# Optimization experiments

Measured on AMD Instinct MI355X. Metric: run time of the kernel, lower is better.

## Reference

```python
import jax, jax.numpy as jnp
import numpy as np

BIG_NUMBER = 1e7   # repo constant used to mask padded adjacency slots
MAX_ITERS = 32     # params['flow_iters']


def _build_graph(B, N, D, valid_deg, seed=0):
    """Random d-regular-ish graph: each valid slot d holds a permutation of nodes,
    so every node has exactly `valid_deg` in-edges. in_indices[b,v,d] = (b,u,s)
    such that adj[b,u,s] == v. Padded slots (d >= valid_deg) hold the sentinel N
    and their in_indices point to a padded (near-zero-weight) flow entry."""
    rng = np.random.default_rng(seed)
    adj = np.full((B, N, D), N, dtype=np.int32)
    in_idx = np.zeros((B, N, D, 3), dtype=np.int32)
    in_idx[..., 0] = np.arange(B, dtype=np.int32)[:, None, None]
    in_idx[..., 2] = valid_deg  # padded slots -> flow[b, 0, valid_deg] (weight ~ 0)
    for b in range(B):
        for d in range(valid_deg):
            perm = rng.permutation(N).astype(np.int32)
            adj[b, :, d] = perm                      # edge u -> perm[u] via slot d
            inv = np.argsort(perm).astype(np.int32)  # inv[v] = u with perm[u] == v
            in_idx[b, :, d, 1] = inv
            in_idx[b, :, d, 2] = d
    return jnp.asarray(adj), jnp.asarray(in_idx)


def setup_inputs():
    B, N, D, VALID = 4, 100000, 16, 12
    key = jax.random.key(0)
    k1, k2 = jax.random.split(key)
    adj_lst, in_indices = _build_graph(B, N, D, VALID)
    return {
        "flow_proportions": jax.random.normal(k1, (B, N, D), dtype=jnp.float32),
        "demands": jax.random.normal(k2, (B, N, 1), dtype=jnp.float32),
        "adj_lst": adj_lst,
        "in_indices": in_indices,
        "num_nodes": N,
    }


def reference(flow_proportions, demands, adj_lst, in_indices, num_nodes):
    # --- masked softmax over neighbor slots (padded slots get -BIG_NUMBER) ---
    mask = (adj_lst == num_nodes).astype(flow_proportions.dtype)   # [B,N,D]
    masked = flow_proportions - BIG_NUMBER * mask
    weights = jax.nn.softmax(masked, axis=-1)                      # normalized_weights

    # --- mcf_solver: iterate flow <- weights * relu(inflow - demand) ---
    bidx = in_indices[..., 0]   # [B,N,D] batch index
    src = in_indices[..., 1]    # [B,N,D] source node of d-th in-edge
    slot = in_indices[..., 2]   # [B,N,D] slot of this node in source's adj list

    def step(flow, _):
        # gather incoming edge flows, sum -> inflow per node [B,N,1]
        inflow = flow[bidx, src, slot].sum(axis=-1, keepdims=True)
        new_flow = weights * jax.nn.relu(inflow - demands)
        return new_flow, None

    flow, _ = jax.lax.scan(step, jnp.zeros_like(weights), None, length=MAX_ITERS)
    # flow_cost (loss) = sum over nodes/slots of cost_fn(flow) = flow**2 here:
    # flow_cost = jnp.sum(flow * flow, axis=(1, 2))
    return flow
```

## Files before the change

kernel.cpp:

```cpp
#include <hip/hip_runtime.h>

#define DEG 16
#define E12 12
#define MAX_ITERS 32
#define BLK 1024
#define LDSF 25600
#define JMAX 96

typedef float f32x4 __attribute__((ext_vector_type(4)));

__device__ __forceinline__ float ld_sc0(const float* p) {
    return __hip_atomic_load((float*)p, __ATOMIC_RELAXED, __HIP_MEMORY_SCOPE_AGENT);
}
__device__ __forceinline__ void st_sc0(float* p, float v) {
    __hip_atomic_store(p, v, __ATOMIC_RELAXED, __HIP_MEMORY_SCOPE_AGENT);
}
__device__ __forceinline__ unsigned ld_u32_sc0(const unsigned* p) {
    return __hip_atomic_load((unsigned*)p, __ATOMIC_RELAXED, __HIP_MEMORY_SCOPE_AGENT);
}
__device__ __forceinline__ void st_u32_sc0(unsigned* p, unsigned v) {
    __hip_atomic_store(p, v, __ATOMIC_RELAXED, __HIP_MEMORY_SCOPE_AGENT);
}

__device__ __forceinline__ f32x4 ld4_nw(const f32x4* p) {
    f32x4 v;
    asm volatile("global_load_dwordx4 %0, %1, off sc0" : "=v"(v) : "v"(p));
    return v;
}
__device__ __forceinline__ float ld1_l2(const float* p) {
    float v;
    asm volatile("global_load_dword %0, %1, off sc0\n\ts_waitcnt vmcnt(0)"
                 : "=v"(v) : "v"(p) : "memory");
    return v;
}
__device__ __forceinline__ void wait_vm0() {
    asm volatile("s_waitcnt vmcnt(0)" ::: "memory");
    __builtin_amdgcn_sched_barrier(0);
}

__device__ __forceinline__ int get_xcd() {
    unsigned x;
    asm volatile("s_getreg_b32 %0, hwreg(HW_REG_XCC_ID)" : "=s"(x));
    return (int)(x & 7u);
}

__device__ __forceinline__ void grid_barrier(unsigned* cnt, unsigned* gen,
                                             unsigned target, unsigned nblocks) {
    __syncthreads();
    if (threadIdx.x == 0) {
        __threadfence();
        unsigned arrived = __hip_atomic_fetch_add(cnt, 1u, __ATOMIC_ACQ_REL,
                                                  __HIP_MEMORY_SCOPE_AGENT);
        if (arrived == nblocks - 1u) {
            __hip_atomic_store(cnt, 0u, __ATOMIC_RELAXED, __HIP_MEMORY_SCOPE_AGENT);
            __hip_atomic_fetch_add(gen, 1u, __ATOMIC_RELEASE, __HIP_MEMORY_SCOPE_AGENT);
        } else {
            while (__hip_atomic_load(gen, __ATOMIC_RELAXED,
                                     __HIP_MEMORY_SCOPE_AGENT) < target)
                __builtin_amdgcn_s_sleep(2);
        }
        __threadfence();
    }
    __syncthreads();
}

__device__ __forceinline__ void xcd_barrier(unsigned* cnt, unsigned* gen,
                                            unsigned target, unsigned nblocks) {
    __syncthreads();
    if (threadIdx.x == 0) {
        unsigned arrived = __hip_atomic_fetch_add(cnt, 1u, __ATOMIC_RELEASE,
                                                  __HIP_MEMORY_SCOPE_WORKGROUP);
        if (arrived == nblocks - 1u) {
            __hip_atomic_store(cnt, 0u, __ATOMIC_RELAXED,
                               __HIP_MEMORY_SCOPE_WORKGROUP);
            __hip_atomic_fetch_add(gen, 1u, __ATOMIC_RELEASE,
                                   __HIP_MEMORY_SCOPE_WORKGROUP);
        } else {
            while (ld_u32_sc0(gen) < target)
                __builtin_amdgcn_s_sleep(2);
        }
    }
    __syncthreads();
}

__device__ __forceinline__ void softmax_row(const float* __restrict__ fp,
                                            const int* __restrict__ adj,
                                            float* __restrict__ wout,
                                            size_t base, int N) {
    const float4* f4 = (const float4*)(fp + base);
    const int4*   a4 = (const int4*)(adj + base);
    float v[DEG];
#pragma unroll
    for (int k = 0; k < DEG / 4; ++k) {
        float4 f = f4[k];
        int4   a = a4[k];
        v[4*k+0] = (a.x == N) ? f.x - 1e7f : f.x;
        v[4*k+1] = (a.y == N) ? f.y - 1e7f : f.y;
        v[4*k+2] = (a.z == N) ? f.z - 1e7f : f.z;
        v[4*k+3] = (a.w == N) ? f.w - 1e7f : f.w;
    }
    float m = v[0];
#pragma unroll
    for (int j = 1; j < DEG; ++j) m = fmaxf(m, v[j]);
    float s = 0.f;
#pragma unroll
    for (int j = 0; j < DEG; ++j) { v[j] = __expf(v[j] - m); s += v[j]; }
    float inv = 1.f / s;
    float4* w4 = (float4*)(wout + base);
#pragma unroll
    for (int k = 0; k < DEG / 4; ++k) {
        float4 o;
        o.x = v[4*k+0] * inv;
        o.y = v[4*k+1] * inv;
        o.z = v[4*k+2] * inv;
        o.w = v[4*k+3] * inv;
        w4[k] = o;
    }
}

__device__ __forceinline__ float node_acc12(const int* __restrict__ es,
                                            const float* __restrict__ ew,
                                            const float* __restrict__ Rc) {
    const int4*   s4 = (const int4*)es;
    const float4* w4 = (const float4*)ew;
    int4 a = s4[0], b = s4[1], c = s4[2];
    float4 x = w4[0], y = w4[1], z = w4[2];
    float acc;
    acc  = x.x * Rc[a.x];  acc += x.y * Rc[a.y];
    acc += x.z * Rc[a.z];  acc += x.w * Rc[a.w];
    acc += y.x * Rc[b.x];  acc += y.y * Rc[b.y];
    acc += y.z * Rc[b.z];  acc += y.w * Rc[b.w];
    acc += z.x * Rc[c.x];  acc += z.y * Rc[c.y];
    acc += z.z * Rc[c.z];  acc += z.w * Rc[c.w];
    return acc;
}

__device__ __forceinline__ void scale_row(float* __restrict__ wout, int g, float r) {
    float4* w4 = (float4*)(wout + (size_t)g * DEG);
#pragma unroll
    for (int k = 0; k < DEG / 4; ++k) {
        float4 v = w4[k];
        v.x *= r; v.y *= r; v.z *= r; v.w *= r;
        w4[k] = v;
    }
}

__global__ __launch_bounds__(BLK, 4)
void fused9_k(const float* __restrict__ fp, const int* __restrict__ adj,
              const int* __restrict__ in_idx, const float* __restrict__ dem,
              const int* __restrict__ nn, float* __restrict__ wout,
              char* __restrict__ wsb, int nodes) {
    __shared__ __align__(16) float lds[LDSF];
    __shared__ int s_xcd, s_rank, s_mode, s_part, s_jbad;
    __shared__ int s_cm[4];
    __shared__ int s_off[5];

    unsigned* g_cnt  = (unsigned*)(wsb);
    unsigned* g_gen  = (unsigned*)(wsb + 128);
    unsigned* blkcnt = (unsigned*)(wsb + 2304);
    unsigned* ovf    = (unsigned*)(wsb + 2432);
    unsigned* jovf   = (unsigned*)(wsb + 2436);
    int*   e_src   = (int*)(wsb + 4096);
    float* e_w     = (float*)(wsb + 4096 + (size_t)nodes * E12 * 4);
    float* Rf0     = (float*)((char*)e_w + (size_t)nodes * E12 * 4);
    float* Rf1     = Rf0 + nodes;
    float* slices  = Rf1 + nodes;
    uint2* regions = (uint2*)((char*)(slices) + (size_t)nodes * 16);

    const int N   = *nn;
    const int tid = (int)threadIdx.x;
    const int T   = (int)gridDim.x * BLK;
    const unsigned nblocks = gridDim.x;
    unsigned gb = 0;

    if (tid == 0) {
        int x = get_xcd();
        s_xcd  = x;
        s_rank = (int)__hip_atomic_fetch_add(&blkcnt[x], 1u, __ATOMIC_RELAXED,
                                             __HIP_MEMORY_SCOPE_AGENT);
    }
    __syncthreads();
    const int my_xcd  = s_xcd;
    const int my_rank = s_rank;

#pragma unroll
    for (int rep = 0; rep < 2; ++rep) {
        int g = (int)blockIdx.x * BLK + tid + rep * T;
        if (g < nodes) softmax_row(fp, adj, wout, (size_t)g * DEG, N);
    }
    grid_barrier(g_cnt, g_gen, ++gb, nblocks);

#pragma unroll
    for (int rep = 0; rep < 2; ++rep) {
        int g = (int)blockIdx.x * BLK + tid + rep * T;
        if (g >= nodes) continue;
        const int gbat = g / N;
        const int4* t4 = (const int4*)(in_idx + (size_t)g * 48);
        int cb[16], cs[16], cl[16];
#pragma unroll
        for (int q = 0; q < 4; ++q) {
            int4 qa = t4[3*q + 0];
            int4 qb = t4[3*q + 1];
            int4 qc = t4[3*q + 2];
            cb[4*q+0] = qa.x; cs[4*q+0] = qa.y; cl[4*q+0] = qa.z;
            cb[4*q+1] = qa.w; cs[4*q+1] = qb.x; cl[4*q+1] = qb.y;
            cb[4*q+2] = qb.z; cs[4*q+2] = qb.w; cl[4*q+2] = qc.x;
            cb[4*q+3] = qc.y; cs[4*q+3] = qc.z; cl[4*q+3] = qc.w;
        }
        float cw[16];
#pragma unroll
        for (int k = 0; k < 16; ++k)
            cw[k] = wout[((size_t)cb[k] * N + cs[k]) * DEG + cl[k]];
        bool bad = (cw[12] != 0.f) || (cw[13] != 0.f) ||
                   (cw[14] != 0.f) || (cw[15] != 0.f);
#pragma unroll
        for (int k = 0; k < E12; ++k)
            bad = bad || (cb[k] != gbat) || ((unsigned)cs[k] >= (unsigned)N);
        if (bad) st_u32_sc0(ovf, 1u);
        int4*   es4 = (int4*)(e_src + (size_t)g * E12);
        float4* ew4 = (float4*)(e_w + (size_t)g * E12);
        es4[0] = make_int4(cs[0], cs[1], cs[2], cs[3]);
        es4[1] = make_int4(cs[4], cs[5], cs[6], cs[7]);
        es4[2] = make_int4(cs[8], cs[9], cs[10], cs[11]);
        ew4[0] = make_float4(cw[0], cw[1], cw[2], cw[3]);
        ew4[1] = make_float4(cw[4], cw[5], cw[6], cw[7]);
        ew4[2] = make_float4(cw[8], cw[9], cw[10], cw[11]);
    }
    grid_barrier(g_cnt, g_gen, ++gb, nblocks);

    const int npb   = (N + 31) >> 5;
    const int nch   = (N + LDSF - 1) / LDSF;
    const int chunk = (N + nch - 1) / nch;
    if (tid == 0) {
        unsigned cc[8];
#pragma unroll
        for (int x = 0; x < 8; ++x) cc[x] = ld_u32_sc0(&blkcnt[x]);
        bool ok = (4 * N == nodes) && (N > 0) && (npb <= 4 * BLK) &&
                  (nch >= 1) && (nch <= 4) && (chunk <= LDSF) &&
                  (ld_u32_sc0(ovf) == 0u);
#pragma unroll
        for (int p = 0; p < 4; ++p)
            ok = ok && (cc[2*p] >= 32u || cc[2*p+1] >= 32u);
        s_mode = ok ? 1 : 0;
        s_part = (ok && cc[my_xcd] >= 32u && my_rank < 32) ? 1 : 0;
    }
    __syncthreads();
    const bool fast = (s_mode == 1);
    const bool part = (s_part == 1);

    if (fast) {
        const int batch = my_xcd >> 1;
        const int lbase = my_rank * npb;
        const int lim   = min(lbase + npb, N);
        float d[4];
        int   lno[4];
        bool  act[4];
        float r[4];
        unsigned mycnt = 0;
        uint2* reg = regions + (size_t)(my_xcd * 32 + my_rank) * (JMAX * BLK);

        if (part) {
            if (tid < 4) s_cm[tid] = 0;
            __syncthreads();
            const int b1 = chunk, b2 = 2 * chunk, b3 = 3 * chunk;
            int c0 = 0, c1 = 0, c2 = 0, c3 = 0;
#pragma unroll
            for (int s = 0; s < 4; ++s) {
                int l = lbase + s * BLK + tid;
                lno[s] = l;
                act[s] = (l < lim);
                d[s] = 0.f;
                if (act[s]) {
                    int g = batch * N + l;
                    d[s] = dem[g];
                    const int* es = e_src + (size_t)g * E12;
#pragma unroll
                    for (int k = 0; k < E12; ++k) {
                        int src = es[k];
                        int c = (src >= b1) + (src >= b2) + (src >= b3);
                        c0 += (c == 0); c1 += (c == 1);
                        c2 += (c == 2); c3 += (c == 3);
                    }
                }
            }
            atomicMax(&s_cm[0], c0); atomicMax(&s_cm[1], c1);
            atomicMax(&s_cm[2], c2); atomicMax(&s_cm[3], c3);
            __syncthreads();
            if (tid == 0) {
                s_off[0] = 0;
                s_off[1] = s_cm[0];
                s_off[2] = s_cm[0] + s_cm[1];
                s_off[3] = s_cm[0] + s_cm[1] + s_cm[2];
                s_off[4] = s_cm[0] + s_cm[1] + s_cm[2] + s_cm[3];
                if (s_off[4] > JMAX) st_u32_sc0(jovf, 1u);
            }
            __syncthreads();
            if (s_off[4] <= JMAX) {
                int cur0 = s_off[0], cur1 = s_off[1],
                    cur2 = s_off[2], cur3 = s_off[3];
#pragma unroll
                for (int s = 0; s < 4; ++s) {
                    if (!act[s]) continue;
                    int g = batch * N + lno[s];
                    const int*   es = e_src + (size_t)g * E12;
                    const float* ew = e_w + (size_t)g * E12;
#pragma unroll
                    for (int k = 0; k < E12; ++k) {
                        int src = es[k];
                        float w = ew[k];
                        int c = (src >= b1) + (src >= b2) + (src >= b3);
                        int j = (c == 0) ? cur0 : (c == 1) ? cur1
                               : (c == 2) ? cur2 : cur3;
                        reg[(size_t)j * BLK + tid] =
                            make_uint2((unsigned)src | ((unsigned)s << 20),
                                       __float_as_uint(w));
                        cur0 += (c == 0); cur1 += (c == 1);
                        cur2 += (c == 2); cur3 += (c == 3);
                    }
                }
                mycnt = (unsigned)(cur0 - s_off[0])
                      | ((unsigned)(cur1 - s_off[1]) << 8)
                      | ((unsigned)(cur2 - s_off[2]) << 16)
                      | ((unsigned)(cur3 - s_off[3]) << 24);
            }
        }
        grid_barrier(g_cnt, g_gen, ++gb, nblocks);
        if (tid == 0) s_jbad = (int)ld_u32_sc0(jovf);
        __syncthreads();

        if (s_jbad == 0) {
            if (!part) return;
            unsigned* xc = (unsigned*)(wsb + 256 + my_xcd * 256);
            unsigned* xg = (unsigned*)(wsb + 256 + my_xcd * 256 + 128);
            unsigned xb = 0;
            float* bufA = slices + (size_t)(2 * my_xcd + 0) * N;
            float* bufB = slices + (size_t)(2 * my_xcd + 1) * N;

#pragma unroll
            for (int s = 0; s < 4; ++s) {
                r[s] = fmaxf(-d[s], 0.f);
                if (act[s]) bufA[lno[s]] = r[s];
            }
            xcd_barrier(xc, xg, ++xb, 32u);

            const uint2* rp = reg + tid;
            float* Rin  = bufA;
            float* Rout = bufB;

#define PROC(PR)                                                       \
            {                                                          \
                float w_ = __uint_as_float((PR).y);                    \
                int idx_ = (int)((PR).x & 0xFFFFFu) - cbase;           \
                int tg_  = (int)((PR).x >> 20);                        \
                float wv_ = w_ * lds[idx_];                            \
                a0 += (tg_ == 0) ? wv_ : 0.f;                          \
                a1 += (tg_ == 1) ? wv_ : 0.f;                          \
                a2 += (tg_ == 2) ? wv_ : 0.f;                          \
                a3 += (tg_ == 3) ? wv_ : 0.f;                          \
            }

            for (int t = 1; t < MAX_ITERS; ++t) {
                float a0 = 0.f, a1 = 0.f, a2 = 0.f, a3 = 0.f;
                for (int c = 0; c < nch; ++c) {
                    const int cbase = c * chunk;
                    const int ce = min(chunk, N - cbase);
                    const float* src = Rin + cbase;
                    if ((((size_t)src) & 15) == 0) {
                        const int n4 = ce >> 2;
                        f32x4* lds4 = (f32x4*)lds;
                        const f32x4* s4 = (const f32x4*)src;
                        f32x4 pv[7];
#pragma unroll
                        for (int k = 0; k < 7; ++k) {
                            int i4 = tid + k * BLK;
                            if (i4 < n4) pv[k] = ld4_nw(s4 + i4);
                        }
                        wait_vm0();
#pragma unroll
                        for (int k = 0; k < 7; ++k) {
                            int i4 = tid + k * BLK;
                            if (i4 < n4) lds4[i4] = pv[k];
                        }
                        for (int i = (n4 << 2) + tid; i < ce; i += BLK)
                            lds[i] = ld1_l2(src + i);
                    } else {
                        for (int i = tid; i < ce; i += BLK)
                            lds[i] = ld1_l2(src + i);
                    }
                    __syncthreads();
                    const int jb = s_off[c];
                    const int je = jb + (int)((mycnt >> (8 * c)) & 255u);
                    int j = jb;
                    for (; j + 4 <= je; j += 4) {
                        uint2 p0 = rp[(size_t)(j + 0) * BLK];
                        uint2 p1 = rp[(size_t)(j + 1) * BLK];
                        uint2 p2 = rp[(size_t)(j + 2) * BLK];
                        uint2 p3 = rp[(size_t)(j + 3) * BLK];
                        PROC(p0); PROC(p1); PROC(p2); PROC(p3);
                    }
                    for (; j < je; ++j) {
                        uint2 pr = rp[(size_t)j * BLK];
                        PROC(pr);
                    }
                    __syncthreads();
                }
                r[0] = fmaxf(a0 - d[0], 0.f);
                r[1] = fmaxf(a1 - d[1], 0.f);
                r[2] = fmaxf(a2 - d[2], 0.f);
                r[3] = fmaxf(a3 - d[3], 0.f);
                if (t < MAX_ITERS - 1) {
#pragma unroll
                    for (int s = 0; s < 4; ++s)
                        if (act[s]) Rout[lno[s]] = r[s];
                    xcd_barrier(xc, xg, ++xb, 32u);
                    float* tmp = Rin; Rin = Rout; Rout = tmp;
                }
            }
#undef PROC
#pragma unroll
            for (int s = 0; s < 4; ++s)
                if (act[s]) scale_row(wout, batch * N + lno[s], r[s]);
            return;
        }
    }

    {
        int g0 = (int)blockIdx.x * BLK + tid;
        int g1 = g0 + T;
        bool a0 = (g0 < nodes), a1 = (g1 < nodes);
        float d0 = a0 ? dem[g0] : 0.f;
        float d1 = a1 ? dem[g1] : 0.f;
        int base0 = a0 ? (g0 / N) * N : 0;
        int base1 = a1 ? (g1 / N) * N : 0;
        float r0 = fmaxf(-d0, 0.f), r1 = fmaxf(-d1, 0.f);
        if (a0) Rf0[g0] = r0;
        if (a1) Rf0[g1] = r1;
        grid_barrier(g_cnt, g_gen, ++gb, nblocks);
        const float* Rc = Rf0;
        float*       Rn = Rf1;
        for (int t = 1; t < MAX_ITERS; ++t) {
            if (a0) r0 = fmaxf(node_acc12(e_src + (size_t)g0 * E12,
                                          e_w + (size_t)g0 * E12,
                                          Rc + base0) - d0, 0.f);
            if (a1) r1 = fmaxf(node_acc12(e_src + (size_t)g1 * E12,
                                          e_w + (size_t)g1 * E12,
                                          Rc + base1) - d1, 0.f);
            if (t < MAX_ITERS - 1) {
                if (a0) Rn[g0] = r0;
                if (a1) Rn[g1] = r1;
                grid_barrier(g_cnt, g_gen, ++gb, nblocks);
                float* tmp = (float*)Rc; Rc = Rn; Rn = tmp;
            }
        }
        if (a0) scale_row(wout, g0, r0);
        if (a1) scale_row(wout, g1, r1);
    }
}

__global__ void softmax_k(const float* __restrict__ fp, const int* __restrict__ adj,
                          const int* __restrict__ nn, float* __restrict__ wout,
                          int nodes) {
    int i = blockIdx.x * blockDim.x + threadIdx.x;
    if (i >= nodes) return;
    softmax_row(fp, adj, wout, (size_t)i * DEG, *nn);
}

__global__ void gather_k(const int* __restrict__ in_idx, const float* __restrict__ w,
                         const int* __restrict__ nn, int* __restrict__ e_srcO,
                         float* __restrict__ e_wO, int edges) {
    int e = blockIdx.x * blockDim.x + threadIdx.x;
    if (e >= edges) return;
    const int N = *nn;
    size_t e3 = 3 * (size_t)e;
    int fi = in_idx[e3] * N + in_idx[e3 + 1];
    e_srcO[e] = fi;
    e_wO[e]   = w[(size_t)fi * DEG + in_idx[e3 + 2]];
}

__global__ void iter_k(const int* __restrict__ e_srcO, const float* __restrict__ e_wO,
                       const float* __restrict__ dem, const float* __restrict__ Rin,
                       float* __restrict__ Rout, int nodes) {
    int i = blockIdx.x * blockDim.x + threadIdx.x;
    if (i >= nodes) return;
    const size_t base = (size_t)i * DEG;
    const int4*   s4 = (const int4*)(e_srcO + base);
    const float4* w4 = (const float4*)(e_wO + base);
    float acc = 0.f;
#pragma unroll
    for (int k = 0; k < DEG / 4; ++k) {
        int4   s = s4[k];
        float4 w = w4[k];
        acc += w.x * Rin[s.x];
        acc += w.y * Rin[s.y];
        acc += w.z * Rin[s.z];
        acc += w.w * Rin[s.w];
    }
    float r = acc - dem[i];
    Rout[i] = r > 0.f ? r : 0.f;
}

__global__ void final_k(const float* __restrict__ w, const float* __restrict__ R,
                        float* __restrict__ out, int nodes) {
    int i = blockIdx.x * blockDim.x + threadIdx.x;
    if (i >= nodes) return;
    scale_row((float*)w, i, R[i]);
    (void)out;
}

extern "C" void kernel_launch(void* const* d_in, const int* in_sizes, int n_in,
                              void* d_out, int out_size, void* d_ws, size_t ws_size,
                              hipStream_t stream) {
    const float* fp  = (const float*)d_in[0];
    const float* dem = (const float*)d_in[1];
    const int*   adj = (const int*)d_in[2];
    const int*   idx = (const int*)d_in[3];
    const int*   nn  = (const int*)d_in[4];

    const int edges = in_sizes[0];
    const int nodes = in_sizes[1];

    float* weights = (float*)d_out;
    char*  ws      = (char*)d_ws;

    int dev = 0, cus = 0, maxBlk = 0;
    hipGetDevice(&dev);
    hipDeviceGetAttribute(&cus, hipDeviceAttributeMultiprocessorCount, dev);
    hipOccupancyMaxActiveBlocksPerMultiprocessor(&maxBlk, (const void*)fused9_k,
                                                 BLK, 0);

    const size_t need = 4096 + (size_t)nodes * (E12 * 8 + 8 + 16)
                      + (size_t)256 * JMAX * BLK * 8;
    const int grid = cus;

    const bool fused_ok = (maxBlk >= 1) && (cus >= 16) &&
                          ((long long)grid * BLK * 2 >= nodes) &&
                          (ws_size >= need) && (nodes % 4 == 0);

    if (fused_ok) {
        hipMemsetAsync(ws, 0, 4096, stream);
        void* args[] = { (void*)&fp, (void*)&adj, (void*)&idx, (void*)&dem,
                         (void*)&nn, (void*)&weights, (void*)&ws, (void*)&nodes };
        hipLaunchCooperativeKernel((const void*)fused9_k, dim3(grid), dim3(BLK),
                                   args, 0, stream);
    } else {
        int*   e_srcO = (int*)ws;
        float* e_wO   = (float*)(ws + (size_t)edges * sizeof(int));
        float* R0     = (float*)(ws + (size_t)edges * 8);
        float* R1     = R0 + nodes;
        const int blk = 256;
        const int gn = (nodes + blk - 1) / blk;
        const int ge = (edges + blk - 1) / blk;
        hipMemsetAsync(R0, 0, (size_t)nodes * sizeof(float), stream);
        softmax_k<<<gn, blk, 0, stream>>>(fp, adj, nn, weights, nodes);
        gather_k<<<ge, blk, 0, stream>>>(idx, weights, nn, e_srcO, e_wO, edges);
        float* a = R0;
        float* b = R1;
        for (int t = 0; t < MAX_ITERS; ++t) {
            iter_k<<<gn, blk, 0, stream>>>(e_srcO, e_wO, dem, a, b, nodes);
            float* tmp = a; a = b; b = tmp;
        }
        final_k<<<gn, blk, 0, stream>>>(weights, a, (float*)d_out, nodes);
    }
}
```

Before: 1.026 ms.

## Double-buffer LDS staging of residual chunks to overlap loads with gather

Splits the per-iteration residual vector into five smaller chunks held in two LDS buffers, so the global loads for the next chunk are issued before gathering from the current one and written to the other buffer afterwards. This aims to hide the global-to-LDS staging latency that was previously serialized with compute, at the cost of one more chunk pass (more partition bookkeeping and a 64-bit count word) and more in-flight registers. It also drops the unaligned-source fallback by requiring N divisible by 4 and rounding the chunk size up to a multiple of 4.

Measured after the change: 1.025 ms. Within noise of the previous version (-0.1%).

```diff
diff --git a/kernel.cpp b/kernel.cpp
--- a/kernel.cpp
+++ b/kernel.cpp
@@ -4,16 +4,14 @@
 #define E12 12
 #define MAX_ITERS 32
 #define BLK 1024
-#define LDSF 25600
+#define NCH 5
+#define LDSH 20000
 #define JMAX 96
 
 typedef float f32x4 __attribute__((ext_vector_type(4)));
 
 __device__ __forceinline__ float ld_sc0(const float* p) {
     return __hip_atomic_load((float*)p, __ATOMIC_RELAXED, __HIP_MEMORY_SCOPE_AGENT);
-}
-__device__ __forceinline__ void st_sc0(float* p, float v) {
-    __hip_atomic_store(p, v, __ATOMIC_RELAXED, __HIP_MEMORY_SCOPE_AGENT);
 }
 __device__ __forceinline__ unsigned ld_u32_sc0(const unsigned* p) {
     return __hip_atomic_load((unsigned*)p, __ATOMIC_RELAXED, __HIP_MEMORY_SCOPE_AGENT);
@@ -145,15 +143,38 @@
     }
 }
 
+__device__ __forceinline__ void stage_issue(const float* src, int ce, int tid,
+                                            f32x4* pv) {
+    const int n4 = ce >> 2;
+    const f32x4* s4 = (const f32x4*)src;
+#pragma unroll
+    for (int k = 0; k < 5; ++k) {
+        int i4 = tid + k * BLK;
+        if (i4 < n4) pv[k] = ld4_nw(s4 + i4);
+    }
+}
+__device__ __forceinline__ void stage_write(float* L, const float* src, int ce,
+                                            int tid, const f32x4* pv) {
+    const int n4 = ce >> 2;
+    f32x4* l4 = (f32x4*)L;
+#pragma unroll
+    for (int k = 0; k < 5; ++k) {
+        int i4 = tid + k * BLK;
+        if (i4 < n4) l4[i4] = pv[k];
+    }
+    for (int i = (n4 << 2) + tid; i < ce; i += BLK)
+        L[i] = ld1_l2(src + i);
+}
+
 __global__ __launch_bounds__(BLK, 4)
-void fused9_k(const float* __restrict__ fp, const int* __restrict__ adj,
-              const int* __restrict__ in_idx, const float* __restrict__ dem,
-              const int* __restrict__ nn, float* __restrict__ wout,
-              char* __restrict__ wsb, int nodes) {
-    __shared__ __align__(16) float lds[LDSF];
+void fused10_k(const float* __restrict__ fp, const int* __restrict__ adj,
+               const int* __restrict__ in_idx, const float* __restrict__ dem,
+               const int* __restrict__ nn, float* __restrict__ wout,
+               char* __restrict__ wsb, int nodes) {
+    __shared__ __align__(16) float lds2[2][LDSH];
     __shared__ int s_xcd, s_rank, s_mode, s_part, s_jbad;
-    __shared__ int s_cm[4];
-    __shared__ int s_off[5];
+    __shared__ int s_cm[NCH];
+    __shared__ int s_off[NCH + 1];
 
     unsigned* g_cnt  = (unsigned*)(wsb);
     unsigned* g_gen  = (unsigned*)(wsb + 128);
@@ -229,14 +250,13 @@
     grid_barrier(g_cnt, g_gen, ++gb, nblocks);
 
     const int npb   = (N + 31) >> 5;
-    const int nch   = (N + LDSF - 1) / LDSF;
-    const int chunk = (N + nch - 1) / nch;
+    const int chunk = (((N + NCH - 1) / NCH) + 3) & ~3;
     if (tid == 0) {
         unsigned cc[8];
 #pragma unroll
         for (int x = 0; x < 8; ++x) cc[x] = ld_u32_sc0(&blkcnt[x]);
-        bool ok = (4 * N == nodes) && (N > 0) && (npb <= 4 * BLK) &&
-                  (nch >= 1) && (nch <= 4) && (chunk <= LDSF) &&
+        bool ok = (4 * N == nodes) && (N > 0) && (N % 4 == 0) &&
+                  (npb <= 4 * BLK) && (chunk <= LDSH) &&
                   (ld_u32_sc0(ovf) == 0u);
 #pragma unroll
         for (int p = 0; p < 4; ++p)
@@ -256,14 +276,14 @@
         int   lno[4];
         bool  act[4];
         float r[4];
-        unsigned mycnt = 0;
+        unsigned long long mycnt = 0;
         uint2* reg = regions + (size_t)(my_xcd * 32 + my_rank) * (JMAX * BLK);
 
         if (part) {
-            if (tid < 4) s_cm[tid] = 0;
+            if (tid < NCH) s_cm[tid] = 0;
             __syncthreads();
-            const int b1 = chunk, b2 = 2 * chunk, b3 = 3 * chunk;
-            int c0 = 0, c1 = 0, c2 = 0, c3 = 0;
+            const int b1 = chunk, b2 = 2 * chunk, b3 = 3 * chunk, b4 = 4 * chunk;
+            int c0 = 0, c1 = 0, c2 = 0, c3 = 0, c4 = 0;
 #pragma unroll
             for (int s = 0; s < 4; ++s) {
                 int l = lbase + s * BLK + tid;
@@ -277,27 +297,27 @@
 #pragma unroll
                     for (int k = 0; k < E12; ++k) {
                         int src = es[k];
-                        int c = (src >= b1) + (src >= b2) + (src >= b3);
-                        c0 += (c == 0); c1 += (c == 1);
-                        c2 += (c == 2); c3 += (c == 3);
+                        int c = (src >= b1) + (src >= b2) + (src >= b3) +
+                                (src >= b4);
+                        c0 += (c == 0); c1 += (c == 1); c2 += (c == 2);
+                        c3 += (c == 3); c4 += (c == 4);
                     }
                 }
             }
             atomicMax(&s_cm[0], c0); atomicMax(&s_cm[1], c1);
             atomicMax(&s_cm[2], c2); atomicMax(&s_cm[3], c3);
+            atomicMax(&s_cm[4], c4);
             __syncthreads();
             if (tid == 0) {
                 s_off[0] = 0;
-                s_off[1] = s_cm[0];
-                s_off[2] = s_cm[0] + s_cm[1];
-                s_off[3] = s_cm[0] + s_cm[1] + s_cm[2];
-                s_off[4] = s_cm[0] + s_cm[1] + s_cm[2] + s_cm[3];
-                if (s_off[4] > JMAX) st_u32_sc0(jovf, 1u);
+#pragma unroll
+                for (int c = 0; c < NCH; ++c) s_off[c + 1] = s_off[c] + s_cm[c];
+                if (s_off[NCH] > JMAX) st_u32_sc0(jovf, 1u);
             }
             __syncthreads();
-            if (s_off[4] <= JMAX) {
-                int cur0 = s_off[0], cur1 = s_off[1],
-                    cur2 = s_off[2], cur3 = s_off[3];
+            if (s_off[NCH] <= JMAX) {
+                int cur0 = s_off[0], cur1 = s_off[1], cur2 = s_off[2],
+                    cur3 = s_off[3], cur4 = s_off[4];
 #pragma unroll
                 for (int s = 0; s < 4; ++s) {
                     if (!act[s]) continue;
@@ -308,20 +328,22 @@
                     for (int k = 0; k < E12; ++k) {
                         int src = es[k];
                         float w = ew[k];
-                        int c = (src >= b1) + (src >= b2) + (src >= b3);
+                        int c = (src >= b1) + (src >= b2) + (src >= b3) +
+                                (src >= b4);
                         int j = (c == 0) ? cur0 : (c == 1) ? cur1
-                               : (c == 2) ? cur2 : cur3;
+                               : (c == 2) ? cur2 : (c == 3) ? cur3 : cur4;
                         reg[(size_t)j * BLK + tid] =
                             make_uint2((unsigned)src | ((unsigned)s << 20),
                                        __float_as_uint(w));
-                        cur0 += (c == 0); cur1 += (c == 1);
-                        cur2 += (c == 2); cur3 += (c == 3);
+                        cur0 += (c == 0); cur1 += (c == 1); cur2 += (c == 2);
+                        cur3 += (c == 3); cur4 += (c == 4);
                     }
                 }
-                mycnt = (unsigned)(cur0 - s_off[0])
-                      | ((unsigned)(cur1 - s_off[1]) << 8)
-                      | ((unsigned)(cur2 - s_off[2]) << 16)
-                      | ((unsigned)(cur3 - s_off[3]) << 24);
+                mycnt = (unsigned long long)(unsigned)(cur0 - s_off[0])
+                      | ((unsigned long long)(unsigned)(cur1 - s_off[1]) << 8)
+                      | ((unsigned long long)(unsigned)(cur2 - s_off[2]) << 16)
+                      | ((unsigned long long)(unsigned)(cur3 - s_off[3]) << 24)
+                      | ((unsigned long long)(unsigned)(cur4 - s_off[4]) << 32);
             }
         }
         grid_barrier(g_cnt, g_gen, ++gb, nblocks);
@@ -352,7 +374,7 @@
                 float w_ = __uint_as_float((PR).y);                    \
                 int idx_ = (int)((PR).x & 0xFFFFFu) - cbase;           \
                 int tg_  = (int)((PR).x >> 20);                        \
-                float wv_ = w_ * lds[idx_];                            \
+                float wv_ = w_ * L[idx_];                              \
                 a0 += (tg_ == 0) ? wv_ : 0.f;                          \
                 a1 += (tg_ == 1) ? wv_ : 0.f;                          \
                 a2 += (tg_ == 2) ? wv_ : 0.f;                          \
@@ -361,35 +383,23 @@
 
             for (int t = 1; t < MAX_ITERS; ++t) {
                 float a0 = 0.f, a1 = 0.f, a2 = 0.f, a3 = 0.f;
-                for (int c = 0; c < nch; ++c) {
+                f32x4 pv[5];
+                {
+                    const int ce0 = min(chunk, N);
+                    stage_issue(Rin, ce0, tid, pv);
+                    wait_vm0();
+                    stage_write(lds2[0], Rin, ce0, tid, pv);
+                }
+                __syncthreads();
+                for (int c = 0; c < NCH; ++c) {
                     const int cbase = c * chunk;
-                    const int ce = min(chunk, N - cbase);
-                    const float* src = Rin + cbase;
-                    if ((((size_t)src) & 15) == 0) {
-                        const int n4 = ce >> 2;
-                        f32x4* lds4 = (f32x4*)lds;
-                        const f32x4* s4 = (const f32x4*)src;
-                        f32x4 pv[7];
-#pragma unroll
-                        for (int k = 0; k < 7; ++k) {
-                            int i4 = tid + k * BLK;
-                            if (i4 < n4) pv[k] = ld4_nw(s4 + i4);
-                        }
-                        wait_vm0();
-#pragma unroll
-                        for (int k = 0; k < 7; ++k) {
-                            int i4 = tid + k * BLK;
-                            if (i4 < n4) lds4[i4] = pv[k];
-                        }
-                        for (int i = (n4 << 2) + tid; i < ce; i += BLK)
-                            lds[i] = ld1_l2(src + i);
-                    } else {
-                        for (int i = tid; i < ce; i += BLK)
-                            lds[i] = ld1_l2(src + i);
-                    }
-                    __syncthreads();
+                    const float* L = lds2[c & 1];
+                    const bool more = (c + 1 < NCH);
+                    const float* src1 = Rin + (c + 1) * chunk;
+                    const int ce1 = more ? min(chunk, N - (c + 1) * chunk) : 0;
+                    if (more) stage_issue(src1, ce1, tid, pv);
                     const int jb = s_off[c];
-                    const int je = jb + (int)((mycnt >> (8 * c)) & 255u);
+                    const int je = jb + (int)((mycnt >> (8 * c)) & 255ull);
                     int j = jb;
                     for (; j + 4 <= je; j += 4) {
                         uint2 p0 = rp[(size_t)(j + 0) * BLK];
@@ -401,6 +411,10 @@
                     for (; j < je; ++j) {
                         uint2 pr = rp[(size_t)j * BLK];
                         PROC(pr);
+                    }
+                    if (more) {
+                        wait_vm0();
+                        stage_write((float*)lds2[(c + 1) & 1], src1, ce1, tid, pv);
                     }
                     __syncthreads();
                 }
@@ -525,7 +539,7 @@
     int dev = 0, cus = 0, maxBlk = 0;
     hipGetDevice(&dev);
     hipDeviceGetAttribute(&cus, hipDeviceAttributeMultiprocessorCount, dev);
-    hipOccupancyMaxActiveBlocksPerMultiprocessor(&maxBlk, (const void*)fused9_k,
+    hipOccupancyMaxActiveBlocksPerMultiprocessor(&maxBlk, (const void*)fused10_k,
                                                  BLK, 0);
 
     const size_t need = 4096 + (size_t)nodes * (E12 * 8 + 8 + 16)
@@ -540,7 +554,7 @@
         hipMemsetAsync(ws, 0, 4096, stream);
         void* args[] = { (void*)&fp, (void*)&adj, (void*)&idx, (void*)&dem,
                          (void*)&nn, (void*)&weights, (void*)&ws, (void*)&nodes };
-        hipLaunchCooperativeKernel((const void*)fused9_k, dim3(grid), dim3(BLK),
+        hipLaunchCooperativeKernel((const void*)fused10_k, dim3(grid), dim3(BLK),
                                    args, 0, stream);
     } else {
         int*   e_srcO = (int*)ws;
```
